# Optimization experiments

Hardware: AMD Instinct MI355X
Metric: run time of the kernel (lower is better)

## Reference

```python
import jax, jax.numpy as jnp
import numpy as np

EMBED_DIM = 1024
HEAD_SIZE = 64
N_HEAD = 16
N_QUERY_GROUPS = 4
SEQ_LEN = 2048
BATCH = 8


def setup_inputs() -> dict:
    key = jax.random.key(0)
    ks = jax.random.split(key, 7)
    s = 1.0 / np.sqrt(EMBED_DIM)
    x = jax.random.normal(ks[0], (BATCH, SEQ_LEN, EMBED_DIM), dtype=jnp.float32)
    Wq = jax.random.uniform(ks[1], (EMBED_DIM, N_HEAD * HEAD_SIZE), jnp.float32, -s, s)
    bq = jax.random.uniform(ks[2], (N_HEAD * HEAD_SIZE,), jnp.float32, -s, s)
    Wk = jax.random.uniform(ks[3], (EMBED_DIM, N_QUERY_GROUPS * HEAD_SIZE), jnp.float32, -s, s)
    bk = jax.random.uniform(ks[4], (N_QUERY_GROUPS * HEAD_SIZE,), jnp.float32, -s, s)
    Wv = jax.random.uniform(ks[5], (EMBED_DIM, N_QUERY_GROUPS * HEAD_SIZE), jnp.float32, -s, s)
    bv = jax.random.uniform(ks[6], (N_QUERY_GROUPS * HEAD_SIZE,), jnp.float32, -s, s)
    return {"x": x, "Wq": Wq, "bq": bq, "Wk": Wk, "bk": bk, "Wv": Wv, "bv": bv}


def reference(x, Wq, bq, Wk, bk, Wv, bv):
    B, T, _ = x.shape
    rep = N_HEAD // N_QUERY_GROUPS  # queries per group
    Q = x @ Wq + bq  # (B, T, H*hs)
    # GQA: torch .repeat tiles the group-block [g0..g3, g0..g3, ...]
    K = (x @ Wk + bk).reshape(B, T, N_QUERY_GROUPS, HEAD_SIZE)
    K = jnp.tile(K, (1, 1, rep, 1)).reshape(B, T, N_HEAD * HEAD_SIZE)
    V = (x @ Wv + bv).reshape(B, T, N_QUERY_GROUPS, HEAD_SIZE)
    V = jnp.tile(V, (1, 1, rep, 1)).reshape(B, T, N_HEAD * HEAD_SIZE)
    # flattened-head scores: contract over full H*hs dim (as in source)
    att = jnp.einsum('btd,bsd->bts', Q, K)  # (B, T, T)
    causal = jnp.triu(jnp.ones((T, T), dtype=bool), k=1)
    mask = jnp.where(causal, jnp.float32(-jnp.inf), jnp.float32(0.0))[None, None]  # (1,1,T,T)
    att = att + mask  # broadcasts to (1, B, T, T), matching torch semantics
    att = jax.nn.softmax(att, axis=-1) / jnp.sqrt(jnp.float32(HEAD_SIZE))  # post-hoc scale, as in source
    out = jnp.einsum('xbts,bsd->xbtd', att, V)  # (1, B, T, H*hs)
    return out
```

## Files before the change

### kernel.cpp

```cpp
#include <hip/hip_runtime.h>
#include <float.h>
#include <stdint.h>

#define T_ 2048
#define DG 256

typedef _Float16 half8 __attribute__((ext_vector_type(8)));
typedef _Float16 half4v __attribute__((ext_vector_type(4)));
typedef __fp16 fp16x2 __attribute__((ext_vector_type(2)));
typedef float f32x4 __attribute__((ext_vector_type(4)));
typedef float f32x16 __attribute__((ext_vector_type(16)));
typedef unsigned uint2v __attribute__((ext_vector_type(2)));

__device__ __forceinline__ void gload16(const void* g, void* l) {
  __builtin_amdgcn_global_load_lds(
      (const __attribute__((address_space(1))) unsigned int*)g,
      (__attribute__((address_space(3))) unsigned int*)l, 16, 0, 0);
}
#define WAIT_VMC(N)  do { asm volatile("s_waitcnt vmcnt(" #N ")" ::: "memory"); __builtin_amdgcn_sched_barrier(0); } while (0)
#define WAIT_LGKM0() do { asm volatile("s_waitcnt lgkmcnt(0)" ::: "memory"); __builtin_amdgcn_sched_barrier(0); } while (0)

__device__ __forceinline__ float cross32(float x, int g) {
  unsigned u = __builtin_bit_cast(unsigned, x);
  uint2v r = __builtin_amdgcn_permlane32_swap(u, u, false, false);
  return __builtin_bit_cast(float, g ? r[0] : r[1]);
}

__global__ __launch_bounds__(256) void prep_w(
    const float* __restrict__ Wq, const float* __restrict__ bq,
    const float* __restrict__ Wk, const float* __restrict__ bk,
    const float* __restrict__ Wv, const float* __restrict__ bv,
    _Float16* __restrict__ Wt, float* __restrict__ bcat) {
  int idx = blockIdx.x * 256 + threadIdx.x;
  int n = idx >> 10, k = idx & 1023;
  float v;
  if (n < 256)      v = Wq[k * 1024 + n] + Wq[k * 1024 + n + 256]
                      + Wq[k * 1024 + n + 512] + Wq[k * 1024 + n + 768];
  else if (n < 512) v = Wk[k * 256 + n - 256];
  else              v = Wv[k * 256 + n - 512];
  Wt[idx] = (_Float16)v;
  if (k == 0) {
    float bb;
    if (n < 256)      bb = bq[n] + bq[n + 256] + bq[n + 512] + bq[n + 768];
    else if (n < 512) bb = bk[n - 256];
    else              bb = bv[n - 512];
    bcat[n] = bb;
  }
}

__global__ __launch_bounds__(256) void qkv_gemm(
    const float* __restrict__ x, const _Float16* __restrict__ Wt,
    const float* __restrict__ bcat,
    _Float16* __restrict__ Qh, _Float16* __restrict__ Kh, _Float16* __restrict__ Vf) {
  __shared__ __align__(16) uint8_t smem[65536];
  const int tid = threadIdx.x;
  const int w = tid >> 6, l = tid & 63;
  const int wr = w >> 1, wc = w & 1;
  const int lr = l & 15, lk = l >> 4;
  const int m0 = blockIdx.x * 128;
  const int by = blockIdx.y;
  const int n0 = by * 256;

  f32x4 acc[4][8] = {};

  auto stage = [&](int k0, int buf) {
    uint8_t* Ab = smem + buf * 32768;
    uint8_t* Bb = Ab + 16384;
#pragma unroll
    for (int i = 0; i < 4; ++i) {
      int si = i * 256 + tid;
      int row = si >> 3, p = si & 7;
      gload16(x + (size_t)(m0 + row) * 1024 + k0 + ((p ^ (row & 7)) << 2), Ab + si * 16);
    }
#pragma unroll
    for (int i = 0; i < 4; ++i) {
      int si = i * 256 + tid;
      int row = si >> 2, p = si & 3;
      gload16(Wt + (size_t)(n0 + row) * 1024 + k0 + ((p ^ (row & 3)) << 3), Bb + si * 16);
    }
  };

  stage(0, 0);
  __syncthreads();

  for (int kt = 0; kt < 32; ++kt) {
    int cur = kt & 1;
    if (kt < 31) stage((kt + 1) * 32, cur ^ 1);
    const uint8_t* Ab = smem + cur * 32768;
    const uint8_t* Bb = Ab + 16384;
    half8 af[4], bf[8];
#pragma unroll
    for (int mi = 0; mi < 4; ++mi) {
      int row = wr * 64 + mi * 16 + lr;
      const float* pa = (const float*)(Ab + row * 128);
      f32x4 a0 = *(const f32x4*)(pa + ((((lk << 1))     ^ (row & 7)) << 2));
      f32x4 a1 = *(const f32x4*)(pa + ((((lk << 1) | 1) ^ (row & 7)) << 2));
      half8 h;
#pragma unroll
      for (int j = 0; j < 4; ++j) { h[j] = (_Float16)a0[j]; h[j + 4] = (_Float16)a1[j]; }
      af[mi] = h;
    }
#pragma unroll
    for (int ni = 0; ni < 8; ++ni) {
      int row = wc * 128 + ni * 16 + lr;
      bf[ni] = *(const half8*)(Bb + row * 64 + ((lk ^ (row & 3)) << 4));
    }
#pragma unroll
    for (int mi = 0; mi < 4; ++mi)
#pragma unroll
      for (int ni = 0; ni < 8; ++ni)
        acc[mi][ni] = __builtin_amdgcn_mfma_f32_16x16x32_f16(af[mi], bf[ni], acc[mi][ni], 0, 0, 0);
    __syncthreads();
  }

#pragma unroll
  for (int mi = 0; mi < 4; ++mi) {
#pragma unroll
    for (int ni = 0; ni < 8; ++ni) {
      int nl = wc * 128 + ni * 16 + lr;
      int mg = m0 + wr * 64 + mi * 16 + lk * 4;
      float bias = bcat[n0 + nl];
      if (by == 0) {
#pragma unroll
        for (int r = 0; r < 4; ++r)
          Qh[(size_t)(mg + r) * DG + nl] = (_Float16)((acc[mi][ni][r] + bias) * 1.44269504f);
      } else if (by == 1) {
#pragma unroll
        for (int r = 0; r < 4; ++r)
          Kh[(size_t)(mg + r) * DG + nl] = (_Float16)(acc[mi][ni][r] + bias);
      } else {
        int dt = nl >> 5, lnv = nl & 31;
        int bb = mg >> 11, t0 = mg & 2047;
        int st = t0 >> 5, sp = t0 & 31;
        int hs = sp >> 4, gg = (sp >> 3) & 1, j0 = sp & 7;
        size_t idx = (size_t)(((bb * 64 + st) * 8 + dt) * 2 + hs) * 512
                   + (gg * 32 + lnv) * 8 + j0;
        half4v h;
#pragma unroll
        for (int r = 0; r < 4; ++r) h[r] = (_Float16)(acc[mi][ni][r] + bias);
        *(half4v*)(Vf + idx) = h;
      }
    }
  }
}

__global__ __launch_bounds__(256, 3) void attn_mfma(
    const _Float16* __restrict__ Qg, const _Float16* __restrict__ Kg,
    const _Float16* __restrict__ Vf, float* __restrict__ out) {
  __shared__ __align__(16) uint8_t smem[49152];
  const int tid = threadIdx.x;
  const int wv = tid >> 6;
  const int l  = tid & 63;
  const int g  = l >> 5;
  const int ln = l & 31;
  const int bid = blockIdx.x;
  const int b   = bid & 7;
  const int tile = (bid < 256) ? (63 - (bid >> 3)) : ((bid - 256) >> 3);
  const int q0 = tile * 32;

  const _Float16* Kb  = Kg + (size_t)b * T_ * DG;
  const _Float16* Vfb = Vf + (size_t)b * 524288;
  float* Sx = (float*)(smem + 32768);

  const _Float16* Qrow = Qg + ((size_t)(b * T_ + q0 + ln)) * DG + wv * 64 + 8 * g;
  half8 qf[4];
#pragma unroll
  for (int j = 0; j < 4; ++j) qf[j] = *(const half8*)(Qrow + j * 16);

  f32x16 o0 = {}, o1 = {};
  float m_r = -1e30f, l_r = 0.0f;

  auto stageK = [&](int s0, int buf) {
    uint8_t* Kl = smem + buf * 16384;
#pragma unroll
    for (int i = 0; i < 4; ++i) {
      int si = i * 256 + tid;
      int row = si >> 5, part = si & 31;
      gload16(Kb + (size_t)(s0 + row) * DG + ((part ^ (row & 7)) << 3), Kl + si * 16);
    }
  };

  stageK(0, 0);
  WAIT_VMC(0);
  __builtin_amdgcn_s_barrier();

  for (int kt = 0; kt <= tile; ++kt) {
    int cur = kt & 1;
    const int dt0 = 2 * wv;
    half8 va0 = *(const half8*)(Vfb + (size_t)((kt * 8 + dt0) * 2 + 0) * 512 + l * 8);
    half8 va1 = *(const half8*)(Vfb + (size_t)((kt * 8 + dt0) * 2 + 1) * 512 + l * 8);
    half8 vb0 = *(const half8*)(Vfb + (size_t)((kt * 8 + dt0 + 1) * 2 + 0) * 512 + l * 8);
    half8 vb1 = *(const half8*)(Vfb + (size_t)((kt * 8 + dt0 + 1) * 2 + 1) * 512 + l * 8);

    const uint8_t* Klds = smem + cur * 16384;
    const int xr = (ln & 7) << 4;
    f32x16 s_acc = {};
    __builtin_amdgcn_s_setprio(1);
#pragma unroll
    for (int j = 0; j < 4; ++j) {
      half8 kf = *(const half8*)(Klds + ln * 512 + ((((4 * wv + j) * 32) + 16 * g) ^ xr));
      s_acc = __builtin_amdgcn_mfma_f32_32x32x16_f16(kf, qf[j], s_acc, 0, 0, 0);
    }
    __builtin_amdgcn_s_setprio(0);

#pragma unroll
    for (int r = 0; r < 16; ++r) Sx[wv * 1024 + r * 64 + l] = s_acc[r];
    if (kt < tile) stageK((kt + 1) * 32, cur ^ 1);
    WAIT_LGKM0();
    __builtin_amdgcn_s_barrier();

    float s[16];
#pragma unroll
    for (int r = 0; r < 16; ++r) s[r] = s_acc[r];
#pragma unroll
    for (int wo = 0; wo < 4; ++wo) {
      if (wo == wv) continue;
#pragma unroll
      for (int r = 0; r < 16; ++r) s[r] += Sx[wo * 1024 + r * 64 + l];
    }

    if (kt == tile) {
#pragma unroll
      for (int r = 0; r < 16; ++r) {
        int srow = (r & 3) + 8 * (r >> 2) + 4 * g;
        if (srow > ln) s[r] = -1e30f;
      }
    }
    float pmax = s[0];
#pragma unroll
    for (int r = 1; r < 16; ++r) pmax = fmaxf(pmax, s[r]);
    pmax = fmaxf(pmax, cross32(pmax, g));
    if (!__all(pmax <= m_r + 8.0f)) {
      float mnew = fmaxf(m_r, pmax);
      float sc = __builtin_amdgcn_exp2f(m_r - mnew);
      l_r *= sc;
#pragma unroll
      for (int r = 0; r < 16; ++r) { o0[r] *= sc; o1[r] *= sc; }
      m_r = mnew;
    }
    float p[16]; float psum = 0.0f;
#pragma unroll
    for (int r = 0; r < 16; ++r) { p[r] = __builtin_amdgcn_exp2f(s[r] - m_r); psum += p[r]; }
    l_r += psum + cross32(psum, g);

    unsigned ph[8];
#pragma unroll
    for (int i = 0; i < 8; ++i) {
      fp16x2 t2 = __builtin_amdgcn_cvt_pkrtz(p[2 * i], p[2 * i + 1]);
      ph[i] = __builtin_bit_cast(unsigned, t2);
    }
    union U { unsigned u[4]; half8 h; };
    U f0, f1;
    {
      uint2v r02 = __builtin_amdgcn_permlane32_swap(ph[0], ph[2], false, false);
      uint2v r13 = __builtin_amdgcn_permlane32_swap(ph[1], ph[3], false, false);
      uint2v r46 = __builtin_amdgcn_permlane32_swap(ph[4], ph[6], false, false);
      uint2v r57 = __builtin_amdgcn_permlane32_swap(ph[5], ph[7], false, false);
      f0.u[0] = r02[0]; f0.u[2] = r02[1];
      f0.u[1] = r13[0]; f0.u[3] = r13[1];
      f1.u[0] = r46[0]; f1.u[2] = r46[1];
      f1.u[1] = r57[0]; f1.u[3] = r57[1];
    }

    __builtin_amdgcn_s_setprio(1);
    o0 = __builtin_amdgcn_mfma_f32_32x32x16_f16(va0, f0.h, o0, 0, 0, 0);
    o0 = __builtin_amdgcn_mfma_f32_32x32x16_f16(va1, f1.h, o0, 0, 0, 0);
    o1 = __builtin_amdgcn_mfma_f32_32x32x16_f16(vb0, f0.h, o1, 0, 0, 0);
    o1 = __builtin_amdgcn_mfma_f32_32x32x16_f16(vb1, f1.h, o1, 0, 0, 0);
    __builtin_amdgcn_s_setprio(0);

    WAIT_VMC(0);
    __builtin_amdgcn_s_barrier();
  }

  float inv = 1.0f / (l_r * 8.0f);
  float* chunk = (float*)(smem + wv * 4352);
  float* ob = out + ((size_t)(b * T_ + q0)) * 1024;
#pragma unroll
  for (int dtl = 0; dtl < 2; ++dtl) {
    const f32x16& oo = dtl ? o1 : o0;
    WAIT_LGKM0();
#pragma unroll
    for (int r = 0; r < 16; ++r) {
      int dl = (r & 3) + 8 * (r >> 2) + 4 * g;
      chunk[ln * 33 + dl] = oo[r] * inv;
    }
    WAIT_LGKM0();
#pragma unroll
    for (int rr = 0; rr < 2; ++rr) {
      int qq = (l >> 2) + 16 * rr;
      int cp = (l & 3) * 8;
      float vv[8];
#pragma unroll
      for (int jj = 0; jj < 8; ++jj) vv[jj] = chunk[qq * 33 + cp + jj];
      float4 w0 = make_float4(vv[0], vv[1], vv[2], vv[3]);
      float4 w1 = make_float4(vv[4], vv[5], vv[6], vv[7]);
      float* orow = ob + (size_t)qq * 1024 + (2 * wv + dtl) * 32 + cp;
#pragma unroll
      for (int rep = 0; rep < 4; ++rep) {
        *(float4*)(orow + rep * 256)     = w0;
        *(float4*)(orow + rep * 256 + 4) = w1;
      }
    }
  }
}

extern "C" void kernel_launch(void* const* d_in, const int* in_sizes, int n_in,
                              void* d_out, int out_size, void* d_ws, size_t ws_size,
                              hipStream_t stream) {
  const float* x  = (const float*)d_in[0];
  const float* Wq = (const float*)d_in[1];
  const float* bq = (const float*)d_in[2];
  const float* Wk = (const float*)d_in[3];
  const float* bk = (const float*)d_in[4];
  const float* Wv = (const float*)d_in[5];
  const float* bv = (const float*)d_in[6];
  float* out = (float*)d_out;
  char* ws = (char*)d_ws;
  _Float16* Wt   = (_Float16*)ws;
  float*    bcat = (float*)(ws + 0x180000);
  _Float16* Qh   = (_Float16*)(ws + 0x181000);
  _Float16* Kh   = Qh + (size_t)16384 * 256;
  _Float16* Vf   = Kh + (size_t)16384 * 256;

  prep_w<<<3072, 256, 0, stream>>>(Wq, bq, Wk, bk, Wv, bv, Wt, bcat);
  qkv_gemm<<<dim3(128, 3), 256, 0, stream>>>(x, Wt, bcat, Qh, Kh, Vf);
  attn_mfma<<<512, 256, 0, stream>>>(Qh, Kh, Vf, out);
}
```

Before: 164.5 us.

## Split long causal attention tiles across two blocks and merge partial softmax results

The attention kernel now splits the key range of the 32 longest query tiles per batch into two halves handled by separate blocks. Each half writes unnormalized output plus its running max and sum to a workspace, and a new merge kernel combines them. The aim is to even out the causal workload imbalance and raise occupancy. Alongside this, the score exchange in LDS moves to a padded row layout with vector loads and stores, qkv_gemm block indices are remapped so consecutive blocks spread across XCDs, and prep_w becomes a grid-stride loop. The cost is an extra kernel launch and partial-result traffic through global memory.

After: 164.9 us. No clear change (+0.2%).

```diff
diff --git a/kernel.cpp b/kernel.cpp
--- a/kernel.cpp
+++ b/kernel.cpp
@@ -12,6 +12,8 @@
 typedef float f32x16 __attribute__((ext_vector_type(16)));
 typedef unsigned uint2v __attribute__((ext_vector_type(2)));
 
+#define PSTRIDE 8256
+
 __device__ __forceinline__ void gload16(const void* g, void* l) {
   __builtin_amdgcn_global_load_lds(
       (const __attribute__((address_space(1))) unsigned int*)g,
@@ -31,20 +33,21 @@
     const float* __restrict__ Wk, const float* __restrict__ bk,
     const float* __restrict__ Wv, const float* __restrict__ bv,
     _Float16* __restrict__ Wt, float* __restrict__ bcat) {
-  int idx = blockIdx.x * 256 + threadIdx.x;
-  int n = idx >> 10, k = idx & 1023;
-  float v;
-  if (n < 256)      v = Wq[k * 1024 + n] + Wq[k * 1024 + n + 256]
-                      + Wq[k * 1024 + n + 512] + Wq[k * 1024 + n + 768];
-  else if (n < 512) v = Wk[k * 256 + n - 256];
-  else              v = Wv[k * 256 + n - 512];
-  Wt[idx] = (_Float16)v;
-  if (k == 0) {
-    float bb;
-    if (n < 256)      bb = bq[n] + bq[n + 256] + bq[n + 512] + bq[n + 768];
-    else if (n < 512) bb = bk[n - 256];
-    else              bb = bv[n - 512];
-    bcat[n] = bb;
+  for (int idx = blockIdx.x * 256 + threadIdx.x; idx < 786432; idx += 768 * 256) {
+    int n = idx >> 10, k = idx & 1023;
+    float v;
+    if (n < 256)      v = Wq[k * 1024 + n] + Wq[k * 1024 + n + 256]
+                        + Wq[k * 1024 + n + 512] + Wq[k * 1024 + n + 768];
+    else if (n < 512) v = Wk[k * 256 + n - 256];
+    else              v = Wv[k * 256 + n - 512];
+    Wt[idx] = (_Float16)v;
+    if (k == 0) {
+      float bb;
+      if (n < 256)      bb = bq[n] + bq[n + 256] + bq[n + 512] + bq[n + 768];
+      else if (n < 512) bb = bk[n - 256];
+      else              bb = bv[n - 512];
+      bcat[n] = bb;
+    }
   }
 }
 
@@ -57,8 +60,10 @@
   const int w = tid >> 6, l = tid & 63;
   const int wr = w >> 1, wc = w & 1;
   const int lr = l & 15, lk = l >> 4;
-  const int m0 = blockIdx.x * 128;
-  const int by = blockIdx.y;
+  const int id = blockIdx.x;
+  const int xcd = id & 7, s = id >> 3;
+  const int m0 = (xcd + 8 * (s / 3)) * 128;
+  const int by = s % 3;
   const int n0 = by * 256;
 
   f32x4 acc[4][8] = {};
@@ -144,19 +149,26 @@
   }
 }
 
-__global__ __launch_bounds__(256, 3) void attn_mfma(
+__global__ __launch_bounds__(256, 3) void attn_main(
     const _Float16* __restrict__ Qg, const _Float16* __restrict__ Kg,
-    const _Float16* __restrict__ Vf, float* __restrict__ out) {
-  __shared__ __align__(16) uint8_t smem[49152];
+    const _Float16* __restrict__ Vf, float* __restrict__ out,
+    float* __restrict__ partials) {
+  __shared__ __align__(16) uint8_t smem[53248];
   const int tid = threadIdx.x;
   const int wv = tid >> 6;
   const int l  = tid & 63;
   const int g  = l >> 5;
   const int ln = l & 31;
-  const int bid = blockIdx.x;
-  const int b   = bid & 7;
-  const int tile = (bid < 256) ? (63 - (bid >> 3)) : ((bid - 256) >> 3);
-  const int q0 = tile * 32;
+  const int id = blockIdx.x;
+  const int b  = id & 7;
+  const int u  = id >> 3;
+  int tt, c, nc;
+  if (u < 64) { tt = 63 - (u >> 1); c = u & 1; nc = 2; }
+  else        { tt = 95 - u;        c = 0;     nc = 1; }
+  const int h  = (tt + 1) >> 1;
+  const int lo = (nc == 2 && c == 1) ? h : 0;
+  const int hi = (nc == 2 && c == 0) ? h : tt + 1;
+  const int q0 = tt * 32;
 
   const _Float16* Kb  = Kg + (size_t)b * T_ * DG;
   const _Float16* Vfb = Vf + (size_t)b * 524288;
@@ -180,12 +192,12 @@
     }
   };
 
-  stageK(0, 0);
+  stageK(lo * 32, 0);
   WAIT_VMC(0);
   __builtin_amdgcn_s_barrier();
 
-  for (int kt = 0; kt <= tile; ++kt) {
-    int cur = kt & 1;
+  for (int kt = lo; kt < hi; ++kt) {
+    int cur = (kt - lo) & 1;
     const int dt0 = 2 * wv;
     half8 va0 = *(const half8*)(Vfb + (size_t)((kt * 8 + dt0) * 2 + 0) * 512 + l * 8);
     half8 va1 = *(const half8*)(Vfb + (size_t)((kt * 8 + dt0) * 2 + 1) * 512 + l * 8);
@@ -203,23 +215,31 @@
     }
     __builtin_amdgcn_s_setprio(0);
 
-#pragma unroll
-    for (int r = 0; r < 16; ++r) Sx[wv * 1024 + r * 64 + l] = s_acc[r];
-    if (kt < tile) stageK((kt + 1) * 32, cur ^ 1);
+    {
+      float* myrow = Sx + (wv * 64 + l) * 20;
+#pragma unroll
+      for (int i = 0; i < 4; ++i)
+        *(f32x4*)(myrow + 4 * i) = *(((const f32x4*)&s_acc) + i);
+    }
+    if (kt + 1 < hi) stageK((kt + 1) * 32, cur ^ 1);
     WAIT_LGKM0();
     __builtin_amdgcn_s_barrier();
 
-    float s[16];
-#pragma unroll
-    for (int r = 0; r < 16; ++r) s[r] = s_acc[r];
+    f32x4 sv[4];
+#pragma unroll
+    for (int i = 0; i < 4; ++i) sv[i] = *(((const f32x4*)&s_acc) + i);
 #pragma unroll
     for (int wo = 0; wo < 4; ++wo) {
       if (wo == wv) continue;
-#pragma unroll
-      for (int r = 0; r < 16; ++r) s[r] += Sx[wo * 1024 + r * 64 + l];
-    }
-
-    if (kt == tile) {
+      const float* prow = Sx + (wo * 64 + l) * 20;
+#pragma unroll
+      for (int i = 0; i < 4; ++i) sv[i] += *(const f32x4*)(prow + 4 * i);
+    }
+    float s[16];
+#pragma unroll
+    for (int r = 0; r < 16; ++r) s[r] = sv[r >> 2][r & 3];
+
+    if (kt == tt) {
 #pragma unroll
       for (int r = 0; r < 16; ++r) {
         int srow = (r & 3) + 8 * (r >> 2) + 4 * g;
@@ -273,35 +293,93 @@
     __builtin_amdgcn_s_barrier();
   }
 
-  float inv = 1.0f / (l_r * 8.0f);
   float* chunk = (float*)(smem + wv * 4352);
-  float* ob = out + ((size_t)(b * T_ + q0)) * 1024;
-#pragma unroll
-  for (int dtl = 0; dtl < 2; ++dtl) {
-    const f32x16& oo = dtl ? o1 : o0;
-    WAIT_LGKM0();
-#pragma unroll
-    for (int r = 0; r < 16; ++r) {
-      int dl = (r & 3) + 8 * (r >> 2) + 4 * g;
-      chunk[ln * 33 + dl] = oo[r] * inv;
-    }
-    WAIT_LGKM0();
-#pragma unroll
-    for (int rr = 0; rr < 2; ++rr) {
-      int qq = (l >> 2) + 16 * rr;
-      int cp = (l & 3) * 8;
-      float vv[8];
-#pragma unroll
-      for (int jj = 0; jj < 8; ++jj) vv[jj] = chunk[qq * 33 + cp + jj];
-      float4 w0 = make_float4(vv[0], vv[1], vv[2], vv[3]);
-      float4 w1 = make_float4(vv[4], vv[5], vv[6], vv[7]);
-      float* orow = ob + (size_t)qq * 1024 + (2 * wv + dtl) * 32 + cp;
-#pragma unroll
-      for (int rep = 0; rep < 4; ++rep) {
-        *(float4*)(orow + rep * 256)     = w0;
-        *(float4*)(orow + rep * 256 + 4) = w1;
-      }
-    }
+  if (nc == 1) {
+    float inv = 1.0f / (l_r * 8.0f);
+    float* ob = out + ((size_t)(b * T_ + q0)) * 1024;
+#pragma unroll
+    for (int dtl = 0; dtl < 2; ++dtl) {
+      const f32x16& oo = dtl ? o1 : o0;
+      WAIT_LGKM0();
+#pragma unroll
+      for (int r = 0; r < 16; ++r) {
+        int dl = (r & 3) + 8 * (r >> 2) + 4 * g;
+        chunk[ln * 33 + dl] = oo[r] * inv;
+      }
+      WAIT_LGKM0();
+#pragma unroll
+      for (int rr = 0; rr < 2; ++rr) {
+        int qq = (l >> 2) + 16 * rr;
+        int cp = (l & 3) * 8;
+        float vv[8];
+#pragma unroll
+        for (int jj = 0; jj < 8; ++jj) vv[jj] = chunk[qq * 33 + cp + jj];
+        float4 w0 = make_float4(vv[0], vv[1], vv[2], vv[3]);
+        float4 w1 = make_float4(vv[4], vv[5], vv[6], vv[7]);
+        float* orow = ob + (size_t)qq * 1024 + (2 * wv + dtl) * 32 + cp;
+#pragma unroll
+        for (int rep = 0; rep < 4; ++rep) {
+          *(float4*)(orow + rep * 256)     = w0;
+          *(float4*)(orow + rep * 256 + 4) = w1;
+        }
+      }
+    }
+  } else {
+    float* P = partials + (size_t)((b * 32 + (tt - 32)) * 2 + c) * PSTRIDE;
+#pragma unroll
+    for (int dtl = 0; dtl < 2; ++dtl) {
+      const f32x16& oo = dtl ? o1 : o0;
+      WAIT_LGKM0();
+#pragma unroll
+      for (int r = 0; r < 16; ++r) {
+        int dl = (r & 3) + 8 * (r >> 2) + 4 * g;
+        chunk[ln * 33 + dl] = oo[r];
+      }
+      WAIT_LGKM0();
+#pragma unroll
+      for (int rr = 0; rr < 2; ++rr) {
+        int qq = (l >> 2) + 16 * rr;
+        int cp = (l & 3) * 8;
+        float vv[8];
+#pragma unroll
+        for (int jj = 0; jj < 8; ++jj) vv[jj] = chunk[qq * 33 + cp + jj];
+        float* prow = P + qq * 256 + (2 * wv + dtl) * 32 + cp;
+        *(float4*)prow       = make_float4(vv[0], vv[1], vv[2], vv[3]);
+        *(float4*)(prow + 4) = make_float4(vv[4], vv[5], vv[6], vv[7]);
+      }
+    }
+    if (wv == 0 && l < 32) { P[8192 + l] = m_r; P[8224 + l] = l_r; }
+  }
+}
+
+__global__ __launch_bounds__(256) void attn_merge(
+    const float* __restrict__ partials, float* __restrict__ out) {
+  const int id = blockIdx.x;
+  const int b = id & 7, tt = 32 + (id >> 3);
+  const float* P0 = partials + (size_t)((b * 32 + (tt - 32)) * 2) * PSTRIDE;
+  const float* P1 = P0 + PSTRIDE;
+  const int tid = threadIdx.x;
+  const int row = tid >> 3, cb = tid & 7;
+  float m0 = P0[8192 + row], l0v = P0[8224 + row];
+  float m1 = P1[8192 + row], l1v = P1[8224 + row];
+  float M   = fmaxf(m0, m1);
+  float sc0 = __builtin_amdgcn_exp2f(m0 - M);
+  float sc1 = __builtin_amdgcn_exp2f(m1 - M);
+  float inv = 1.0f / ((l0v * sc0 + l1v * sc1) * 8.0f);
+  const float4* r0 = (const float4*)(P0 + row * 256 + cb * 32);
+  const float4* r1 = (const float4*)(P1 + row * 256 + cb * 32);
+  float* orow = out + ((size_t)(b * T_ + tt * 32 + row)) * 1024 + cb * 32;
+#pragma unroll
+  for (int j = 0; j < 8; ++j) {
+    float4 a = r0[j], bb = r1[j];
+    float4 v;
+    v.x = (a.x * sc0 + bb.x * sc1) * inv;
+    v.y = (a.y * sc0 + bb.y * sc1) * inv;
+    v.z = (a.z * sc0 + bb.z * sc1) * inv;
+    v.w = (a.w * sc0 + bb.w * sc1) * inv;
+#pragma unroll
+    for (int rep = 0; rep < 4; ++rep)
+      *(float4*)(orow + rep * 256 + j * 4) = v;
   }
 }
 
@@ -322,8 +400,10 @@
   _Float16* Qh   = (_Float16*)(ws + 0x181000);
   _Float16* Kh   = Qh + (size_t)16384 * 256;
   _Float16* Vf   = Kh + (size_t)16384 * 256;
-
-  prep_w<<<3072, 256, 0, stream>>>(Wq, bq, Wk, bk, Wv, bv, Wt, bcat);
-  qkv_gemm<<<dim3(128, 3), 256, 0, stream>>>(x, Wt, bcat, Qh, Kh, Vf);
-  attn_mfma<<<512, 256, 0, stream>>>(Qh, Kh, Vf, out);
-}
+  float* partials = (float*)(Vf + (size_t)16384 * 256);
+
+  prep_w<<<768, 256, 0, stream>>>(Wq, bq, Wk, bk, Wv, bv, Wt, bcat);
+  qkv_gemm<<<384, 256, 0, stream>>>(x, Wt, bcat, Qh, Kh, Vf);
+  attn_main<<<768, 256, 0, stream>>>(Qh, Kh, Vf, out, partials);
+  attn_merge<<<256, 256, 0, stream>>>(partials, out);
+}
```
